# Performance work log

Hardware: AMD Instinct MI355X
Metric: run time of the kernel (lower is better)

## Reference

```python
import jax, jax.numpy as jnp
import numpy as np

B, T, D = 32, 512, 256
F = 256  # duration_predictor_filter_size
K = 3    # kernel size, padding=1
MEL_MAX = 2304
EPS = 1e-5


def _conv1d(x, w, b):
    # x: [B, T, C_in], w: [C_out, C_in, K], 'same'-ish padding=1
    y = jax.lax.conv_general_dilated(
        x.transpose(0, 2, 1), w, window_strides=(1,), padding=[(1, 1)],
        dimension_numbers=("NCH", "OIH", "NCH"))
    return y.transpose(0, 2, 1) + b


def _layernorm(x, g, b):
    mu = jnp.mean(x, axis=-1, keepdims=True)
    var = jnp.mean(jnp.square(x - mu), axis=-1, keepdims=True)
    return (x - mu) * jax.lax.rsqrt(var + EPS) * g + b


def setup_inputs() -> dict:
    key = jax.random.key(0)
    ks = jax.random.split(key, 8)
    x = jax.random.normal(ks[0], (B, T, D), dtype=jnp.float32)
    target = jax.random.randint(ks[1], (B, T), 0, 8, dtype=jnp.int32)
    s = 0.02
    return {
        "x": x,
        "target": target,
        "mel_max_length": MEL_MAX,
        "conv1_w": jax.random.normal(ks[2], (F, D, K), dtype=jnp.float32) * s,
        "conv1_b": jnp.zeros((F,), jnp.float32),
        "ln1_g": jnp.ones((F,), jnp.float32),
        "ln1_b": jnp.zeros((F,), jnp.float32),
        "conv2_w": jax.random.normal(ks[3], (F, F, K), dtype=jnp.float32) * s,
        "conv2_b": jnp.zeros((F,), jnp.float32),
        "ln2_g": jnp.ones((F,), jnp.float32),
        "ln2_b": jnp.zeros((F,), jnp.float32),
        "lin_w": jax.random.normal(ks[4], (1, F), dtype=jnp.float32) * s,
        "lin_b": jnp.zeros((1,), jnp.float32),
    }


def reference(x, target, mel_max_length, conv1_w, conv1_b, ln1_g, ln1_b,
              conv2_w, conv2_b, ln2_g, ln2_b, lin_w, lin_b):
    # Variance_adaptor (duration predictor), eval-mode dropout = identity
    h = jax.nn.relu(_layernorm(_conv1d(x, conv1_w, conv1_b), ln1_g, ln1_b))
    h = jax.nn.relu(_layernorm(_conv1d(h, conv2_w, conv2_b), ln2_g, ln2_b))
    dur_pred = jax.nn.relu(jnp.einsum("btf,of->bto", h, lin_w) + lin_b)[..., 0]  # [B,T]

    # LR: alignment @ x, expressed as the equivalent duration-indexed gather.
    # alignment[b, t_out, j] = 1 iff cumsum(dur)[b,j-1] <= t_out < cumsum(dur)[b,j]
    cum = jnp.cumsum(target, axis=1)                    # [B, T]
    t_out = jnp.arange(mel_max_length, dtype=cum.dtype)  # [T_out]
    idx = jax.vmap(lambda c: jnp.searchsorted(c, t_out, side="right"))(cum)  # [B, T_out]
    valid = (t_out[None, :] < cum[:, -1:]).astype(x.dtype)                   # [B, T_out]
    gathered = jnp.take_along_axis(x, jnp.clip(idx, 0, T - 1)[:, :, None], axis=1)
    output = gathered * valid[:, :, None]                # zeros past total length (pad)
    return output, dur_pred
```

## Files before the change

### kernel.cpp

```cpp
#include <hip/hip_runtime.h>

typedef __attribute__((ext_vector_type(8))) short short8;
typedef __attribute__((ext_vector_type(4))) float floatx4;

typedef __attribute__((address_space(3))) unsigned int lds_u32;
typedef __attribute__((address_space(1))) const unsigned int glb_u32;

static __device__ __forceinline__ unsigned short f2bf(float f) {
    unsigned int u = __float_as_uint(f);
    return (unsigned short)((u + 0x7FFFu + ((u >> 16) & 1u)) >> 16);
}
static __device__ __forceinline__ void cp16(const ushort* g, ushort* l) {
    __builtin_amdgcn_global_load_lds((glb_u32*)g, (lds_u32*)l, 16, 0, 0);
}

__global__ __launch_bounds__(256)
void prep_kernel(const float* __restrict__ x, const float* __restrict__ w1,
                 const float* __restrict__ w2,
                 ushort* __restrict__ xb, ushort* __restrict__ h1b,
                 ushort* __restrict__ w1pb, ushort* __restrict__ w2pb)
{
    const int blk = blockIdx.x, tid = threadIdx.x;
    if (blk < 4112) {
        const int r = blk * 4 + (tid >> 6);
        const int c = (tid & 63) * 4;
        const int b = r / 514, tp = r % 514;
        ushort4 o;
        if (tp >= 1 && tp <= 512) {
            float4 v = *(const float4*)(x + ((size_t)(b * 512 + tp - 1) * 256 + c));
            o.x = f2bf(v.x); o.y = f2bf(v.y); o.z = f2bf(v.z); o.w = f2bf(v.w);
        } else {
            o.x = o.y = o.z = o.w = 0;
            *(ushort4*)(h1b + (size_t)r * 256 + c) = o;
        }
        *(ushort4*)(xb + (size_t)r * 256 + c) = o;
    } else {
        const bool second = blk >= 4880;
        const int e = (blk - (second ? 4880 : 4112)) * 256 + tid;
        const float* w = second ? w2 : w1;
        ushort* wpb = second ? w2pb : w1pb;
        const int f = e / 768, j = e % 768;
        const int c = j & 255, kr = j >> 8;
        const int s = j >> 6, kk = j & 63;
        wpb[s * 16384 + f * 64 + (((kk >> 3) ^ (f & 7)) << 3) + (kk & 7)]
            = f2bf(w[f * 768 + c * 3 + kr]);
    }
}

template<bool IS_CONV2>
__global__ __launch_bounds__(256, 2)
void conv_mfma_kernel(const ushort* __restrict__ xb,
                      const ushort* __restrict__ wpb,
                      const float* __restrict__ cbias,
                      const float* __restrict__ gamma, const float* __restrict__ beta,
                      const float* __restrict__ lw, const float* __restrict__ lb,
                      ushort* __restrict__ outb,
                      float* __restrict__ durp,
                      const float* __restrict__ x,
                      const int* __restrict__ target,
                      float* __restrict__ out0)
{
    __shared__ ushort As[32 * 64];
    __shared__ ushort Bs[256 * 64];
    __shared__ float sum_s[4][32], sq_s[4][32], mu_s[32], rs_s[32];
    __shared__ int cum[512], ps[256], sidx[64];

    const int tid = threadIdx.x;

    if (IS_CONV2 && blockIdx.x >= 512) {
        const int bg = blockIdx.x - 512;
        const int b = bg / 36, t0o = (bg % 36) * 64;
        const int v0 = target[b * 512 + 2 * tid];
        const int v1 = target[b * 512 + 2 * tid + 1];
        ps[tid] = v0 + v1;
        __syncthreads();
        for (int off = 1; off < 256; off <<= 1) {
            int t = (tid >= off) ? ps[tid - off] : 0;
            __syncthreads();
            ps[tid] += t;
            __syncthreads();
        }
        const int excl = tid ? ps[tid - 1] : 0;
        cum[2 * tid]     = excl + v0;
        cum[2 * tid + 1] = excl + v0 + v1;
        __syncthreads();
        const int total = cum[511];
        if (tid < 64) {
            int t = t0o + tid;
            int lo = 0, hi = 512;
            while (lo < hi) {
                int mid = (lo + hi) >> 1;
                if (cum[mid] <= t) lo = mid + 1; else hi = mid;
            }
            sidx[tid] = (t < total) ? ((lo < 512) ? lo : 511) : -1;
        }
        __syncthreads();
        const float4* x4 = (const float4*)x;
        float4* o4 = (float4*)out0;
        const int lane6 = tid & 63, g4 = tid >> 6;
        #pragma unroll 4
        for (int rr = 0; rr < 16; ++rr) {
            int r = rr * 4 + g4;
            int idx = sidx[r];
            float4 v = make_float4(0.f, 0.f, 0.f, 0.f);
            if (idx >= 0) v = x4[((size_t)(b * 512 + idx)) * 64 + lane6];
            o4[((size_t)(b * 2304 + t0o + r)) * 64 + lane6] = v;
        }
        return;
    }

    const int w_ = tid >> 6, lane = tid & 63;
    const int q = lane >> 4, col = lane & 15;
    const int b  = blockIdx.x & 31;
    const int t0 = (blockIdx.x >> 5) << 5;
    const int rot = blockIdx.x % 12;

    floatx4 acc[2][4] = {};
    const ushort* xbb = xb + (size_t)b * 514 * 256;
    const int arow = tid >> 3, aquad = (tid & 7) ^ (arow & 7);
    ushort* AsW = As + (size_t)w_ * 512;
    ushort* BsW = Bs + (size_t)w_ * 512;

    for (int s = 0; s < 12; ++s) {
        int se = s + rot; if (se >= 12) se -= 12;
        const int krow = se >> 2, cbo = (se & 3) << 6;
        cp16(xbb + (size_t)(t0 + krow + arow) * 256 + cbo + aquad * 8, AsW);
        const ushort* wsrc = wpb + (size_t)se * 16384 + w_ * 512 + lane * 8;
        #pragma unroll
        for (int i = 0; i < 8; ++i) cp16(wsrc + i * 2048, BsW + i * 2048);
        __syncthreads();
        short8 af[2][2], bf[4][2];
        #pragma unroll
        for (int mi = 0; mi < 2; ++mi)
            #pragma unroll
            for (int kh = 0; kh < 2; ++kh)
                af[mi][kh] = *(const short8*)((const char*)As
                    + (mi * 16 + col) * 128 + (((kh * 4 + q) ^ (col & 7)) * 16));
        #pragma unroll
        for (int ni = 0; ni < 4; ++ni)
            #pragma unroll
            for (int kh = 0; kh < 2; ++kh)
                bf[ni][kh] = *(const short8*)((const char*)Bs
                    + (w_ * 64 + ni * 16 + col) * 128 + (((kh * 4 + q) ^ (col & 7)) * 16));
        #pragma unroll
        for (int kh = 0; kh < 2; ++kh)
            #pragma unroll
            for (int mi = 0; mi < 2; ++mi)
                #pragma unroll
                for (int ni = 0; ni < 4; ++ni)
                    acc[mi][ni] = __builtin_amdgcn_mfma_f32_16x16x32_bf16(
                        af[mi][kh], bf[ni][kh], acc[mi][ni], 0, 0, 0);
        __syncthreads();
    }

    const int base_c = w_ * 64;
    float cb4[4], gm4[4], bt4[4];
    #pragma unroll
    for (int ni = 0; ni < 4; ++ni) {
        cb4[ni] = cbias[base_c + ni * 16 + col];
        gm4[ni] = gamma[base_c + ni * 16 + col];
        bt4[ni] = beta [base_c + ni * 16 + col];
    }
    float rsum[2][4] = {}, rsq[2][4] = {};
    #pragma unroll
    for (int mi = 0; mi < 2; ++mi)
        #pragma unroll
        for (int ni = 0; ni < 4; ++ni)
            #pragma unroll
            for (int r = 0; r < 4; ++r) {
                float v = acc[mi][ni][r] + cb4[ni];
                acc[mi][ni][r] = v;
                rsum[mi][r] += v;
                rsq [mi][r] += v * v;
            }
    #pragma unroll
    for (int mi = 0; mi < 2; ++mi)
        #pragma unroll
        for (int r = 0; r < 4; ++r) {
            float s = rsum[mi][r], ss = rsq[mi][r];
            #pragma unroll
            for (int d = 8; d > 0; d >>= 1) {
                s  += __shfl_down(s,  d, 16);
                ss += __shfl_down(ss, d, 16);
            }
            if (col == 0) {
                sum_s[w_][mi * 16 + q * 4 + r] = s;
                sq_s [w_][mi * 16 + q * 4 + r] = ss;
            }
        }
    __syncthreads();
    if (tid < 32) {
        float s  = sum_s[0][tid] + sum_s[1][tid] + sum_s[2][tid] + sum_s[3][tid];
        float ss = sq_s [0][tid] + sq_s [1][tid] + sq_s [2][tid] + sq_s [3][tid];
        float mu = s * (1.f / 256.f);
        mu_s[tid] = mu;
        rs_s[tid] = rsqrtf(ss * (1.f / 256.f) - mu * mu + 1e-5f);
    }
    __syncthreads();

    if (!IS_CONV2) {
        #pragma unroll
        for (int mi = 0; mi < 2; ++mi)
            #pragma unroll
            for (int ni = 0; ni < 4; ++ni)
                #pragma unroll
                for (int r = 0; r < 4; ++r) {
                    int row = mi * 16 + q * 4 + r;
                    float v = (acc[mi][ni][r] - mu_s[row]) * rs_s[row] * gm4[ni] + bt4[ni];
                    outb[((size_t)b * 514 + t0 + row + 1) * 256 + base_c + ni * 16 + col]
                        = f2bf(fmaxf(v, 0.f));
                }
    } else {
        float lw4[4];
        #pragma unroll
        for (int ni = 0; ni < 4; ++ni) lw4[ni] = lw[base_c + ni * 16 + col];
        float dsum[2][4] = {};
        #pragma unroll
        for (int mi = 0; mi < 2; ++mi)
            #pragma unroll
            for (int ni = 0; ni < 4; ++ni)
                #pragma unroll
                for (int r = 0; r < 4; ++r) {
                    int row = mi * 16 + q * 4 + r;
                    float v = (acc[mi][ni][r] - mu_s[row]) * rs_s[row] * gm4[ni] + bt4[ni];
                    dsum[mi][r] += fmaxf(v, 0.f) * lw4[ni];
                }
        #pragma unroll
        for (int mi = 0; mi < 2; ++mi)
            #pragma unroll
            for (int r = 0; r < 4; ++r) {
                float s = dsum[mi][r];
                #pragma unroll
                for (int d = 8; d > 0; d >>= 1) s += __shfl_down(s, d, 16);
                if (col == 0) sum_s[w_][mi * 16 + q * 4 + r] = s;
            }
        __syncthreads();
        if (tid < 32)
            durp[b * 512 + t0 + tid] = fmaxf(sum_s[0][tid] + sum_s[1][tid]
                                           + sum_s[2][tid] + sum_s[3][tid] + lb[0], 0.f);
    }
}

extern "C" void kernel_launch(void* const* d_in, const int* in_sizes, int n_in,
                              void* d_out, int out_size, void* d_ws, size_t ws_size,
                              hipStream_t stream) {
    const float* x      = (const float*)d_in[0];
    const int*   target = (const int*)  d_in[1];
    const float* c1w = (const float*)d_in[3];
    const float* c1b = (const float*)d_in[4];
    const float* g1  = (const float*)d_in[5];
    const float* b1  = (const float*)d_in[6];
    const float* c2w = (const float*)d_in[7];
    const float* c2b = (const float*)d_in[8];
    const float* g2  = (const float*)d_in[9];
    const float* b2  = (const float*)d_in[10];
    const float* lw  = (const float*)d_in[11];
    const float* lb  = (const float*)d_in[12];

    const size_t PADEL = (size_t)32 * 514 * 256;
    ushort* xb   = (ushort*)d_ws;
    ushort* h1b  = xb + PADEL;
    ushort* w1pb = h1b + PADEL;
    ushort* w2pb = w1pb + 196608;

    float* out0 = (float*)d_out;
    float* durp = out0 + (size_t)32 * 2304 * 256;

    prep_kernel<<<5648, 256, 0, stream>>>(x, c1w, c2w, xb, h1b, w1pb, w2pb);
    conv_mfma_kernel<false><<<512, 256, 0, stream>>>(
        xb, w1pb, c1b, g1, b1, nullptr, nullptr, h1b, nullptr,
        nullptr, nullptr, nullptr);
    conv_mfma_kernel<true><<<512 + 1152, 256, 0, stream>>>(
        h1b, w2pb, c2b, g2, b2, lw, lb, nullptr, durp,
        x, target, out0);
}
```

Measured before the change: 148.0 us.

## Fuse x bf16 conversion into conv1, double-buffer LDS, interleave gather blocks

Removes the padded bf16 copy of x from the prep kernel. Conv1 now reads fp32 x directly, converts it to bf16 in registers and handles the edge padding itself. The K-loop is double-buffered in LDS, so the next stage's weight and activation loads are issued before the current MFMAs. Conv2's gather blocks are interleaved with its conv blocks (4 conv and 9 gather per group of 13) to balance work across the grid. The cost is doubled LDS use, which may reduce occupancy, and conv1 A-tile loads going through registers instead of direct-to-LDS copies.

```diff
diff --git a/kernel.cpp b/kernel.cpp
--- a/kernel.cpp
+++ b/kernel.cpp
@@ -15,28 +15,14 @@
 }
 
 __global__ __launch_bounds__(256)
-void prep_kernel(const float* __restrict__ x, const float* __restrict__ w1,
-                 const float* __restrict__ w2,
-                 ushort* __restrict__ xb, ushort* __restrict__ h1b,
-                 ushort* __restrict__ w1pb, ushort* __restrict__ w2pb)
+void prep_kernel(const float* __restrict__ w1, const float* __restrict__ w2,
+                 ushort* __restrict__ w1pb, ushort* __restrict__ w2pb,
+                 ushort* __restrict__ h1b)
 {
     const int blk = blockIdx.x, tid = threadIdx.x;
-    if (blk < 4112) {
-        const int r = blk * 4 + (tid >> 6);
-        const int c = (tid & 63) * 4;
-        const int b = r / 514, tp = r % 514;
-        ushort4 o;
-        if (tp >= 1 && tp <= 512) {
-            float4 v = *(const float4*)(x + ((size_t)(b * 512 + tp - 1) * 256 + c));
-            o.x = f2bf(v.x); o.y = f2bf(v.y); o.z = f2bf(v.z); o.w = f2bf(v.w);
-        } else {
-            o.x = o.y = o.z = o.w = 0;
-            *(ushort4*)(h1b + (size_t)r * 256 + c) = o;
-        }
-        *(ushort4*)(xb + (size_t)r * 256 + c) = o;
-    } else {
-        const bool second = blk >= 4880;
-        const int e = (blk - (second ? 4880 : 4112)) * 256 + tid;
+    if (blk < 1536) {
+        const bool second = blk >= 768;
+        const int e = (blk - (second ? 768 : 0)) * 256 + tid;
         const float* w = second ? w2 : w1;
         ushort* wpb = second ? w2pb : w1pb;
         const int f = e / 768, j = e % 768;
@@ -44,12 +30,17 @@
         const int s = j >> 6, kk = j & 63;
         wpb[s * 16384 + f * 64 + (((kk >> 3) ^ (f & 7)) << 3) + (kk & 7)]
             = f2bf(w[f * 768 + c * 3 + kr]);
+    } else {
+        const int b = blk - 1536;
+        h1b[((size_t)b * 514 + 0)   * 256 + tid] = 0;
+        h1b[((size_t)b * 514 + 513) * 256 + tid] = 0;
     }
 }
 
 template<bool IS_CONV2>
 __global__ __launch_bounds__(256, 2)
-void conv_mfma_kernel(const ushort* __restrict__ xb,
+void conv_mfma_kernel(const float* __restrict__ xf,
+                      const ushort* __restrict__ xb,
                       const ushort* __restrict__ wpb,
                       const float* __restrict__ cbias,
                       const float* __restrict__ gamma, const float* __restrict__ beta,
@@ -60,87 +51,134 @@
                       const int* __restrict__ target,
                       float* __restrict__ out0)
 {
-    __shared__ ushort As[32 * 64];
-    __shared__ ushort Bs[256 * 64];
+    __shared__ ushort As[2 * 32 * 64];
+    __shared__ ushort Bs[2 * 256 * 64];
     __shared__ float sum_s[4][32], sq_s[4][32], mu_s[32], rs_s[32];
     __shared__ int cum[512], ps[256], sidx[64];
 
     const int tid = threadIdx.x;
-
-    if (IS_CONV2 && blockIdx.x >= 512) {
-        const int bg = blockIdx.x - 512;
-        const int b = bg / 36, t0o = (bg % 36) * 64;
-        const int v0 = target[b * 512 + 2 * tid];
-        const int v1 = target[b * 512 + 2 * tid + 1];
-        ps[tid] = v0 + v1;
-        __syncthreads();
-        for (int off = 1; off < 256; off <<= 1) {
-            int t = (tid >= off) ? ps[tid - off] : 0;
+    int conv_id;
+    if (IS_CONV2) {
+        const int grp = blockIdx.x / 13, rmod = blockIdx.x % 13;
+        if (rmod >= 4) {
+            const int bg = grp * 9 + (rmod - 4);
+            const int b = bg / 36, t0o = (bg % 36) * 64;
+            const int v0 = target[b * 512 + 2 * tid];
+            const int v1 = target[b * 512 + 2 * tid + 1];
+            ps[tid] = v0 + v1;
             __syncthreads();
-            ps[tid] += t;
+            for (int off = 1; off < 256; off <<= 1) {
+                int t = (tid >= off) ? ps[tid - off] : 0;
+                __syncthreads();
+                ps[tid] += t;
+                __syncthreads();
+            }
+            const int excl = tid ? ps[tid - 1] : 0;
+            cum[2 * tid]     = excl + v0;
+            cum[2 * tid + 1] = excl + v0 + v1;
             __syncthreads();
-        }
-        const int excl = tid ? ps[tid - 1] : 0;
-        cum[2 * tid]     = excl + v0;
-        cum[2 * tid + 1] = excl + v0 + v1;
-        __syncthreads();
-        const int total = cum[511];
-        if (tid < 64) {
-            int t = t0o + tid;
-            int lo = 0, hi = 512;
-            while (lo < hi) {
-                int mid = (lo + hi) >> 1;
-                if (cum[mid] <= t) lo = mid + 1; else hi = mid;
-            }
-            sidx[tid] = (t < total) ? ((lo < 512) ? lo : 511) : -1;
-        }
-        __syncthreads();
-        const float4* x4 = (const float4*)x;
-        float4* o4 = (float4*)out0;
-        const int lane6 = tid & 63, g4 = tid >> 6;
-        #pragma unroll 4
-        for (int rr = 0; rr < 16; ++rr) {
-            int r = rr * 4 + g4;
-            int idx = sidx[r];
-            float4 v = make_float4(0.f, 0.f, 0.f, 0.f);
-            if (idx >= 0) v = x4[((size_t)(b * 512 + idx)) * 64 + lane6];
-            o4[((size_t)(b * 2304 + t0o + r)) * 64 + lane6] = v;
-        }
-        return;
+            const int total = cum[511];
+            if (tid < 64) {
+                int t = t0o + tid;
+                int lo = 0, hi = 512;
+                while (lo < hi) {
+                    int mid = (lo + hi) >> 1;
+                    if (cum[mid] <= t) lo = mid + 1; else hi = mid;
+                }
+                sidx[tid] = (t < total) ? ((lo < 512) ? lo : 511) : -1;
+            }
+            __syncthreads();
+            const float4* x4 = (const float4*)x;
+            float4* o4 = (float4*)out0;
+            const int lane6 = tid & 63, g4 = tid >> 6;
+            #pragma unroll 4
+            for (int rr = 0; rr < 16; ++rr) {
+                int r = rr * 4 + g4;
+                int idx = sidx[r];
+                float4 v = make_float4(0.f, 0.f, 0.f, 0.f);
+                if (idx >= 0) v = x4[((size_t)(b * 512 + idx)) * 64 + lane6];
+                o4[((size_t)(b * 2304 + t0o + r)) * 64 + lane6] = v;
+            }
+            return;
+        }
+        conv_id = grp * 4 + rmod;
+    } else {
+        conv_id = blockIdx.x;
     }
 
     const int w_ = tid >> 6, lane = tid & 63;
     const int q = lane >> 4, col = lane & 15;
-    const int b  = blockIdx.x & 31;
-    const int t0 = (blockIdx.x >> 5) << 5;
-    const int rot = blockIdx.x % 12;
+    const int b  = conv_id & 31;
+    const int t0 = (conv_id >> 5) << 5;
+    const int rot = conv_id % 12;
 
     floatx4 acc[2][4] = {};
-    const ushort* xbb = xb + (size_t)b * 514 * 256;
     const int arow = tid >> 3, aquad = (tid & 7) ^ (arow & 7);
-    ushort* AsW = As + (size_t)w_ * 512;
-    ushort* BsW = Bs + (size_t)w_ * 512;
-
+    const ushort* xbb = IS_CONV2 ? (xb + (size_t)b * 514 * 256) : (const ushort*)nullptr;
+    const float*  xfb = IS_CONV2 ? (const float*)nullptr : (xf + (size_t)b * 512 * 256);
+
+    {
+        const int se = rot;
+        const int krow = se >> 2, cbo = (se & 3) << 6;
+        const ushort* wsrc = wpb + (size_t)se * 16384 + w_ * 512 + lane * 8;
+        ushort* dstB = Bs + w_ * 512;
+        #pragma unroll
+        for (int i = 0; i < 8; ++i) cp16(wsrc + i * 2048, dstB + i * 2048);
+        if (IS_CONV2) {
+            cp16(xbb + (size_t)(t0 + krow + arow) * 256 + cbo + aquad * 8, As + w_ * 512);
+        } else {
+            const int row = t0 + krow + arow - 1;
+            float4 av0 = make_float4(0.f, 0.f, 0.f, 0.f), av1 = av0;
+            if (row >= 0 && row < 512) {
+                const float* px = xfb + ((size_t)row * 256 + cbo + aquad * 8);
+                av0 = *(const float4*)px;
+                av1 = *(const float4*)(px + 4);
+            }
+            short8 aval;
+            aval[0] = f2bf(av0.x); aval[1] = f2bf(av0.y);
+            aval[2] = f2bf(av0.z); aval[3] = f2bf(av0.w);
+            aval[4] = f2bf(av1.x); aval[5] = f2bf(av1.y);
+            aval[6] = f2bf(av1.z); aval[7] = f2bf(av1.w);
+            *(short8*)(As + tid * 8) = aval;
+        }
+    }
+    __syncthreads();
+
+    int cur = 0;
     for (int s = 0; s < 12; ++s) {
-        int se = s + rot; if (se >= 12) se -= 12;
-        const int krow = se >> 2, cbo = (se & 3) << 6;
-        cp16(xbb + (size_t)(t0 + krow + arow) * 256 + cbo + aquad * 8, AsW);
-        const ushort* wsrc = wpb + (size_t)se * 16384 + w_ * 512 + lane * 8;
-        #pragma unroll
-        for (int i = 0; i < 8; ++i) cp16(wsrc + i * 2048, BsW + i * 2048);
-        __syncthreads();
+        const int nb = cur ^ 1;
+        float4 av0 = make_float4(0.f, 0.f, 0.f, 0.f), av1 = av0;
+        if (s + 1 < 12) {
+            int sn = s + 1 + rot; if (sn >= 12) sn -= 12;
+            const int krow = sn >> 2, cbo = (sn & 3) << 6;
+            const ushort* wsrc = wpb + (size_t)sn * 16384 + w_ * 512 + lane * 8;
+            ushort* dstB = Bs + (size_t)nb * 16384 + w_ * 512;
+            #pragma unroll
+            for (int i = 0; i < 8; ++i) cp16(wsrc + i * 2048, dstB + i * 2048);
+            if (IS_CONV2) {
+                cp16(xbb + (size_t)(t0 + krow + arow) * 256 + cbo + aquad * 8,
+                     As + (size_t)nb * 2048 + w_ * 512);
+            } else {
+                const int row = t0 + krow + arow - 1;
+                if (row >= 0 && row < 512) {
+                    const float* px = xfb + ((size_t)row * 256 + cbo + aquad * 8);
+                    av0 = *(const float4*)px;
+                    av1 = *(const float4*)(px + 4);
+                }
+            }
+        }
         short8 af[2][2], bf[4][2];
         #pragma unroll
         for (int mi = 0; mi < 2; ++mi)
             #pragma unroll
             for (int kh = 0; kh < 2; ++kh)
-                af[mi][kh] = *(const short8*)((const char*)As
+                af[mi][kh] = *(const short8*)((const char*)As + cur * 4096
                     + (mi * 16 + col) * 128 + (((kh * 4 + q) ^ (col & 7)) * 16));
         #pragma unroll
         for (int ni = 0; ni < 4; ++ni)
             #pragma unroll
             for (int kh = 0; kh < 2; ++kh)
-                bf[ni][kh] = *(const short8*)((const char*)Bs
+                bf[ni][kh] = *(const short8*)((const char*)Bs + cur * 32768
                     + (w_ * 64 + ni * 16 + col) * 128 + (((kh * 4 + q) ^ (col & 7)) * 16));
         #pragma unroll
         for (int kh = 0; kh < 2; ++kh)
@@ -150,7 +188,16 @@
                 for (int ni = 0; ni < 4; ++ni)
                     acc[mi][ni] = __builtin_amdgcn_mfma_f32_16x16x32_bf16(
                         af[mi][kh], bf[ni][kh], acc[mi][ni], 0, 0, 0);
+        if (!IS_CONV2 && s + 1 < 12) {
+            short8 aval;
+            aval[0] = f2bf(av0.x); aval[1] = f2bf(av0.y);
+            aval[2] = f2bf(av0.z); aval[3] = f2bf(av0.w);
+            aval[4] = f2bf(av1.x); aval[5] = f2bf(av1.y);
+            aval[6] = f2bf(av1.z); aval[7] = f2bf(av1.w);
+            *(short8*)(As + (size_t)nb * 2048 + tid * 8) = aval;
+        }
         __syncthreads();
+        cur = nb;
     }
 
     const int base_c = w_ * 64;
@@ -258,19 +305,18 @@
     const float* lb  = (const float*)d_in[12];
 
     const size_t PADEL = (size_t)32 * 514 * 256;
-    ushort* xb   = (ushort*)d_ws;
-    ushort* h1b  = xb + PADEL;
+    ushort* h1b  = (ushort*)d_ws;
     ushort* w1pb = h1b + PADEL;
     ushort* w2pb = w1pb + 196608;
 
     float* out0 = (float*)d_out;
     float* durp = out0 + (size_t)32 * 2304 * 256;
 
-    prep_kernel<<<5648, 256, 0, stream>>>(x, c1w, c2w, xb, h1b, w1pb, w2pb);
+    prep_kernel<<<1568, 256, 0, stream>>>(c1w, c2w, w1pb, w2pb, h1b);
     conv_mfma_kernel<false><<<512, 256, 0, stream>>>(
-        xb, w1pb, c1b, g1, b1, nullptr, nullptr, h1b, nullptr,
+        x, nullptr, w1pb, c1b, g1, b1, nullptr, nullptr, h1b, nullptr,
         nullptr, nullptr, nullptr);
-    conv_mfma_kernel<true><<<512 + 1152, 256, 0, stream>>>(
-        h1b, w2pb, c2b, g2, b2, lw, lb, nullptr, durp,
+    conv_mfma_kernel<true><<<1664, 256, 0, stream>>>(
+        nullptr, h1b, w2pb, c2b, g2, b2, lw, lb, nullptr, durp,
         x, target, out0);
 }
```

Result: slower. 158.5 us (+7.0%).

## Load conv MFMA fragments directly from global and move gather into prep kernel

Applied to the files above, without the earlier changes.

The conv kernel no longer stages A and B tiles through LDS with global_load_lds and block barriers. Each wave now loads its bf16 fragments straight from global memory into registers, double-buffered in software so loads overlap the MFMAs. The weight swizzle is dropped because LDS bank conflicts no longer apply, and occupancy is raised to 3 blocks per SM. The length-regulator gather moves from the conv2 launch into the prep kernel, trading barrier and LDS costs for more global and L2 traffic, since each wave re-reads shared weight data that was previously loaded once per block.

```diff
diff --git a/kernel.cpp b/kernel.cpp
--- a/kernel.cpp
+++ b/kernel.cpp
@@ -2,73 +2,23 @@
 
 typedef __attribute__((ext_vector_type(8))) short short8;
 typedef __attribute__((ext_vector_type(4))) float floatx4;
-
-typedef __attribute__((address_space(3))) unsigned int lds_u32;
-typedef __attribute__((address_space(1))) const unsigned int glb_u32;
 
 static __device__ __forceinline__ unsigned short f2bf(float f) {
     unsigned int u = __float_as_uint(f);
     return (unsigned short)((u + 0x7FFFu + ((u >> 16) & 1u)) >> 16);
 }
-static __device__ __forceinline__ void cp16(const ushort* g, ushort* l) {
-    __builtin_amdgcn_global_load_lds((glb_u32*)g, (lds_u32*)l, 16, 0, 0);
-}
 
 __global__ __launch_bounds__(256)
-void prep_kernel(const float* __restrict__ x, const float* __restrict__ w1,
-                 const float* __restrict__ w2,
+void prep_kernel(const float* __restrict__ x, const int* __restrict__ target,
+                 const float* __restrict__ w1, const float* __restrict__ w2,
                  ushort* __restrict__ xb, ushort* __restrict__ h1b,
-                 ushort* __restrict__ w1pb, ushort* __restrict__ w2pb)
+                 ushort* __restrict__ w1q, ushort* __restrict__ w2q,
+                 float* __restrict__ out0)
 {
+    __shared__ int cum[512], ps[256], sidx[64];
     const int blk = blockIdx.x, tid = threadIdx.x;
-    if (blk < 4112) {
-        const int r = blk * 4 + (tid >> 6);
-        const int c = (tid & 63) * 4;
-        const int b = r / 514, tp = r % 514;
-        ushort4 o;
-        if (tp >= 1 && tp <= 512) {
-            float4 v = *(const float4*)(x + ((size_t)(b * 512 + tp - 1) * 256 + c));
-            o.x = f2bf(v.x); o.y = f2bf(v.y); o.z = f2bf(v.z); o.w = f2bf(v.w);
-        } else {
-            o.x = o.y = o.z = o.w = 0;
-            *(ushort4*)(h1b + (size_t)r * 256 + c) = o;
-        }
-        *(ushort4*)(xb + (size_t)r * 256 + c) = o;
-    } else {
-        const bool second = blk >= 4880;
-        const int e = (blk - (second ? 4880 : 4112)) * 256 + tid;
-        const float* w = second ? w2 : w1;
-        ushort* wpb = second ? w2pb : w1pb;
-        const int f = e / 768, j = e % 768;
-        const int c = j & 255, kr = j >> 8;
-        const int s = j >> 6, kk = j & 63;
-        wpb[s * 16384 + f * 64 + (((kk >> 3) ^ (f & 7)) << 3) + (kk & 7)]
-            = f2bf(w[f * 768 + c * 3 + kr]);
-    }
-}
-
-template<bool IS_CONV2>
-__global__ __launch_bounds__(256, 2)
-void conv_mfma_kernel(const ushort* __restrict__ xb,
-                      const ushort* __restrict__ wpb,
-                      const float* __restrict__ cbias,
-                      const float* __restrict__ gamma, const float* __restrict__ beta,
-                      const float* __restrict__ lw, const float* __restrict__ lb,
-                      ushort* __restrict__ outb,
-                      float* __restrict__ durp,
-                      const float* __restrict__ x,
-                      const int* __restrict__ target,
-                      float* __restrict__ out0)
-{
-    __shared__ ushort As[32 * 64];
-    __shared__ ushort Bs[256 * 64];
-    __shared__ float sum_s[4][32], sq_s[4][32], mu_s[32], rs_s[32];
-    __shared__ int cum[512], ps[256], sidx[64];
-
-    const int tid = threadIdx.x;
-
-    if (IS_CONV2 && blockIdx.x >= 512) {
-        const int bg = blockIdx.x - 512;
+    if (blk < 1152) {
+        const int bg = blk;
         const int b = bg / 36, t0o = (bg % 36) * 64;
         const int v0 = target[b * 512 + 2 * tid];
         const int v1 = target[b * 512 + 2 * tid + 1];
@@ -106,9 +56,44 @@
             if (idx >= 0) v = x4[((size_t)(b * 512 + idx)) * 64 + lane6];
             o4[((size_t)(b * 2304 + t0o + r)) * 64 + lane6] = v;
         }
-        return;
-    }
-
+    } else if (blk < 5264) {
+        const int r = (blk - 1152) * 4 + (tid >> 6);
+        const int c = (tid & 63) * 4;
+        const int b = r / 514, tp = r % 514;
+        ushort4 o;
+        if (tp >= 1 && tp <= 512) {
+            float4 v = *(const float4*)(x + ((size_t)(b * 512 + tp - 1) * 256 + c));
+            o.x = f2bf(v.x); o.y = f2bf(v.y); o.z = f2bf(v.z); o.w = f2bf(v.w);
+        } else {
+            o.x = o.y = o.z = o.w = 0;
+            *(ushort4*)(h1b + (size_t)r * 256 + c) = o;
+        }
+        *(ushort4*)(xb + (size_t)r * 256 + c) = o;
+    } else {
+        const bool second = blk >= 6032;
+        const int e = (blk - (second ? 6032 : 5264)) * 256 + tid;
+        const float* w = second ? w2 : w1;
+        ushort* wq = second ? w2q : w1q;
+        const int f = e / 768, j = e % 768;
+        const int c = j & 255, kr = j >> 8;
+        const int s = j >> 6, kk = j & 63;
+        wq[s * 16384 + f * 64 + kk] = f2bf(w[f * 768 + c * 3 + kr]);
+    }
+}
+
+template<bool IS_CONV2>
+__global__ __launch_bounds__(256, 3)
+void conv_mfma_kernel(const ushort* __restrict__ src,
+                      const ushort* __restrict__ wq,
+                      const float* __restrict__ cbias,
+                      const float* __restrict__ gamma, const float* __restrict__ beta,
+                      const float* __restrict__ lw, const float* __restrict__ lb,
+                      ushort* __restrict__ outb,
+                      float* __restrict__ durp)
+{
+    __shared__ float sum_s[4][32], sq_s[4][32], mu_s[32], rs_s[32];
+
+    const int tid = threadIdx.x;
     const int w_ = tid >> 6, lane = tid & 63;
     const int q = lane >> 4, col = lane & 15;
     const int b  = blockIdx.x & 31;
@@ -116,42 +101,43 @@
     const int rot = blockIdx.x % 12;
 
     floatx4 acc[2][4] = {};
-    const ushort* xbb = xb + (size_t)b * 514 * 256;
-    const int arow = tid >> 3, aquad = (tid & 7) ^ (arow & 7);
-    ushort* AsW = As + (size_t)w_ * 512;
-    ushort* BsW = Bs + (size_t)w_ * 512;
-
-    for (int s = 0; s < 12; ++s) {
-        int se = s + rot; if (se >= 12) se -= 12;
-        const int krow = se >> 2, cbo = (se & 3) << 6;
-        cp16(xbb + (size_t)(t0 + krow + arow) * 256 + cbo + aquad * 8, AsW);
-        const ushort* wsrc = wpb + (size_t)se * 16384 + w_ * 512 + lane * 8;
-        #pragma unroll
-        for (int i = 0; i < 8; ++i) cp16(wsrc + i * 2048, BsW + i * 2048);
-        __syncthreads();
-        short8 af[2][2], bf[4][2];
-        #pragma unroll
-        for (int mi = 0; mi < 2; ++mi)
-            #pragma unroll
-            for (int kh = 0; kh < 2; ++kh)
-                af[mi][kh] = *(const short8*)((const char*)As
-                    + (mi * 16 + col) * 128 + (((kh * 4 + q) ^ (col & 7)) * 16));
-        #pragma unroll
-        for (int ni = 0; ni < 4; ++ni)
-            #pragma unroll
-            for (int kh = 0; kh < 2; ++kh)
-                bf[ni][kh] = *(const short8*)((const char*)Bs
-                    + (w_ * 64 + ni * 16 + col) * 128 + (((kh * 4 + q) ^ (col & 7)) * 16));
-        #pragma unroll
-        for (int kh = 0; kh < 2; ++kh)
-            #pragma unroll
-            for (int mi = 0; mi < 2; ++mi)
-                #pragma unroll
-                for (int ni = 0; ni < 4; ++ni)
-                    acc[mi][ni] = __builtin_amdgcn_mfma_f32_16x16x32_bf16(
-                        af[mi][kh], bf[ni][kh], acc[mi][ni], 0, 0, 0);
-        __syncthreads();
-    }
+
+    const ushort* abase = src + (size_t)b * 514 * 256 + (size_t)(t0 + col) * 256 + q * 8;
+    const ushort* bbase = wq + (size_t)(w_ * 64 + col) * 64 + q * 8;
+
+    short8 afA[2][2], bfA[4][2], afB[2][2], bfB[4][2];
+
+#define LOADF(AF, BF, SE_) do {                                                   \
+        const int se_ = (SE_);                                                    \
+        const int aoff_ = (se_ >> 2) * 256 + ((se_ & 3) << 6);                    \
+        _Pragma("unroll") for (int mi = 0; mi < 2; ++mi)                          \
+        _Pragma("unroll") for (int kh = 0; kh < 2; ++kh)                          \
+            AF[mi][kh] = *(const short8*)(abase + mi * 4096 + kh * 32 + aoff_);   \
+        _Pragma("unroll") for (int ni = 0; ni < 4; ++ni)                          \
+        _Pragma("unroll") for (int kh = 0; kh < 2; ++kh)                          \
+            BF[ni][kh] = *(const short8*)(bbase + ni * 1024 + kh * 32 + se_ * 16384); \
+    } while (0)
+
+#define MFMAS(AF, BF) do {                                                        \
+        _Pragma("unroll") for (int kh = 0; kh < 2; ++kh)                          \
+        _Pragma("unroll") for (int mi = 0; mi < 2; ++mi)                          \
+        _Pragma("unroll") for (int ni = 0; ni < 4; ++ni)                          \
+            acc[mi][ni] = __builtin_amdgcn_mfma_f32_16x16x32_bf16(                \
+                AF[mi][kh], BF[ni][kh], acc[mi][ni], 0, 0, 0);                    \
+    } while (0)
+
+    auto se_of = [&](int s) { int v = s + rot; return v >= 12 ? v - 12 : v; };
+
+    LOADF(afA, bfA, se_of(0));
+    #pragma unroll
+    for (int s = 0; s < 12; s += 2) {
+        LOADF(afB, bfB, se_of(s + 1));
+        MFMAS(afA, bfA);
+        if (s + 2 < 12) LOADF(afA, bfA, se_of(s + 2));
+        MFMAS(afB, bfB);
+    }
+#undef LOADF
+#undef MFMAS
 
     const int base_c = w_ * 64;
     float cb4[4], gm4[4], bt4[4];
@@ -260,17 +246,15 @@
     const size_t PADEL = (size_t)32 * 514 * 256;
     ushort* xb   = (ushort*)d_ws;
     ushort* h1b  = xb + PADEL;
-    ushort* w1pb = h1b + PADEL;
-    ushort* w2pb = w1pb + 196608;
+    ushort* w1q  = h1b + PADEL;
+    ushort* w2q  = w1q + 196608;
 
     float* out0 = (float*)d_out;
     float* durp = out0 + (size_t)32 * 2304 * 256;
 
-    prep_kernel<<<5648, 256, 0, stream>>>(x, c1w, c2w, xb, h1b, w1pb, w2pb);
+    prep_kernel<<<6800, 256, 0, stream>>>(x, target, c1w, c2w, xb, h1b, w1q, w2q, out0);
     conv_mfma_kernel<false><<<512, 256, 0, stream>>>(
-        xb, w1pb, c1b, g1, b1, nullptr, nullptr, h1b, nullptr,
-        nullptr, nullptr, nullptr);
-    conv_mfma_kernel<true><<<512 + 1152, 256, 0, stream>>>(
-        h1b, w2pb, c2b, g2, b2, lw, lb, nullptr, durp,
-        x, target, out0);
-}
+        xb, w1q, c1b, g1, b1, nullptr, nullptr, h1b, nullptr);
+    conv_mfma_kernel<true><<<512, 256, 0, stream>>>(
+        h1b, w2q, c2b, g2, b2, lw, lb, nullptr, durp);
+}
```

New measurement: 189.0 us. 27.7% more time.
